# Kernel tuning notes

Measured on AMD Instinct MI355X. Metric: run time of the kernel, lower is better.

## Reference

```python
import jax, jax.numpy as jnp
import numpy as np

CLAMP = 1.0e6
LN_EPS = 1e-5
TWO_PI = 6.283185307179586


def _layernorm_last(x, gamma, beta):
    mu = jnp.mean(x, axis=-1, keepdims=True)
    var = jnp.var(x, axis=-1, keepdims=True)
    return (x - mu) * jax.lax.rsqrt(var + LN_EPS) * gamma + beta


def _candidates(xc):
    # xc: (C, B, S, D) pre-scaled + clamped input, one slice per candidate
    return jnp.stack([
        xc[0],
        xc[1] * xc[1],
        jnp.cos(TWO_PI * xc[2]),
        jnp.sin(xc[3]),
        jnp.exp(xc[4]),
        jnp.ones_like(xc[5]),
        xc[6] * xc[6] * xc[6],
        jnp.log(jnp.abs(xc[7]) + 1.0),
        jnp.sqrt(jnp.abs(xc[8])),
        jnp.tanh(xc[9]),
    ], axis=0)


def setup_inputs() -> dict:
    key = jax.random.key(0)
    ks = jax.random.split(key, 5)
    B, S, D, C = 4, 2048, 1024, 10
    return {
        "x": jax.random.normal(ks[0], (B, S, D), dtype=jnp.float32),
        "ln_gamma": jnp.ones((D,), dtype=jnp.float32),
        "ln_beta": jnp.zeros((D,), dtype=jnp.float32),
        "log_in_scale": jax.random.normal(ks[1], (C,), dtype=jnp.float32) * 0.05,
        "log_out_scale": jax.random.normal(ks[2], (C,), dtype=jnp.float32) * 0.05,
        "gate_w": jax.random.normal(ks[3], (C, D), dtype=jnp.float32) * (D ** -0.5),
        "gate_b": jnp.zeros((C,), dtype=jnp.float32),
    }


def reference(x, ln_gamma, ln_beta, log_in_scale, log_out_scale, gate_w, gate_b):
    # Input LayerNorm over D
    x_norm = _layernorm_last(x, ln_gamma, ln_beta)  # (B,S,D)

    in_s = jnp.exp(log_in_scale)    # (C,)
    out_s = jnp.exp(log_out_scale)  # (C,)

    # Per-candidate input scale + clamp
    xc = x_norm[None] * in_s[:, None, None, None]          # (C,B,S,D)
    xc = jnp.clip(xc, -CLAMP, CLAMP)

    cand = _candidates(xc) * out_s[:, None, None, None]    # (C,B,S,D)
    cand = jnp.clip(cand, -CLAMP, CLAMP)

    # permute to (B,S,C,D) and LayerNorm jointly over (C,D), no affine
    cand = jnp.transpose(cand, (1, 2, 0, 3))                # (B,S,C,D)
    mu = jnp.mean(cand, axis=(2, 3), keepdims=True)
    var = jnp.var(cand, axis=(2, 3), keepdims=True)
    cand = (cand - mu) * jax.lax.rsqrt(var + LN_EPS)
    cand = jnp.clip(cand, -CLAMP, CLAMP)
    cand = jnp.nan_to_num(cand, nan=0.0, posinf=CLAMP, neginf=-CLAMP)

    # Gate on the RAW input x (as in the torch code), softmax over candidates
    gate_logits = jnp.einsum('bsd,cd->bsc', x, gate_w) + gate_b  # (B,S,C)
    gate_weights = jax.nn.softmax(gate_logits, axis=-1)

    # Weighted sum over the candidate axis
    weighted = jnp.einsum('bsc,bscd->bsd', gate_weights, cand)   # (B,S,D)
    return weighted, gate_weights
```

## Files before the change

### kernel.cpp

```cpp
#include <hip/hip_runtime.h>
#include <math.h>

constexpr int D_DIM = 1024;
constexpr int C_DIM = 10;
constexpr int WPB   = 8;
constexpr int BLOCK = 64 * WPB;

constexpr float CLAMP_V  = 1.0e6f;
constexpr float LOG2E    = 1.4426950408889634f;
constexpr float LN2      = 0.6931471805599453f;
constexpr float INV_2PI  = 0.15915494309189535f;

__device__ __forceinline__ float2 pmul(float2 a, float2 b) {
    return make_float2(a.x * b.x, a.y * b.y);
}
__device__ __forceinline__ float2 pfma(float2 a, float2 b, float2 c) {
    return make_float2(fmaf(a.x, b.x, c.x), fmaf(a.y, b.y, c.y));
}
__device__ __forceinline__ float2 padd(float2 a, float2 b) {
    return make_float2(a.x + b.x, a.y + b.y);
}
__device__ __forceinline__ float2 bc(float s) { return make_float2(s, s); }

__device__ __forceinline__ float rfl(float x) {
    return __int_as_float(__builtin_amdgcn_readfirstlane(__float_as_int(x)));
}

template <int CTRL>
__device__ __forceinline__ float dpp_add(float v) {
    const int s = __builtin_amdgcn_update_dpp(
        0, __float_as_int(v), CTRL, 0xf, 0xf, false);
    return v + __int_as_float(s);
}
__device__ __forceinline__ float wave_sum_sgpr(float v) {
    v = dpp_add<0x111>(v);
    v = dpp_add<0x112>(v);
    v = dpp_add<0x114>(v);
    v = dpp_add<0x118>(v);
    v = dpp_add<0x142>(v);
    v = dpp_add<0x143>(v);
    return __int_as_float(__builtin_amdgcn_readlane(__float_as_int(v), 63));
}

__global__ __launch_bounds__(BLOCK)
void fused_sme_kernel(const float* __restrict__ x,
                      const float* __restrict__ ln_gamma,
                      const float* __restrict__ ln_beta,
                      const float* __restrict__ log_in_scale,
                      const float* __restrict__ log_out_scale,
                      const float* __restrict__ gate_w,
                      const float* __restrict__ gate_b,
                      float* __restrict__ out_weighted,
                      float* __restrict__ out_gate,
                      int tokens)
{
    const int t    = threadIdx.x;
    const int lane = t & 63;
    const int wv   = t >> 6;
    int token = blockIdx.x * WPB + wv;
    token = min(token, tokens - 1);

    __shared__ float gws[C_DIM * D_DIM];

    const float* xrow = x + (size_t)token * D_DIM + (lane << 2);
    float4 xv[4];
#pragma unroll
    for (int k = 0; k < 4; ++k)
        xv[k] = *reinterpret_cast<const float4*>(xrow + k * 256);

#pragma unroll
    for (int i = 0; i < 5; ++i) {
        const int idx = t + i * BLOCK;
        reinterpret_cast<float4*>(gws)[idx] =
            reinterpret_cast<const float4*>(gate_w)[idx];
    }

    float r[12];
    {
        float2 s = bc(0.0f), q = bc(0.0f);
#pragma unroll
        for (int k = 0; k < 4; ++k) {
            const float2 lo = make_float2(xv[k].x, xv[k].y);
            const float2 hi = make_float2(xv[k].z, xv[k].w);
            s = padd(s, padd(lo, hi));
            q = pfma(lo, lo, q);
            q = pfma(hi, hi, q);
        }
        r[0] = wave_sum_sgpr(s.x + s.y);
        r[1] = wave_sum_sgpr(q.x + q.y);
    }

    __syncthreads();

#pragma unroll
    for (int c = 0; c < C_DIM; ++c) {
        const float* gr = gws + c * D_DIM + (lane << 2);
        float2 d2 = bc(0.0f);
#pragma unroll
        for (int k = 0; k < 4; ++k) {
            const float4 gv = *reinterpret_cast<const float4*>(gr + k * 256);
            d2 = pfma(make_float2(xv[k].x, xv[k].y), make_float2(gv.x, gv.y), d2);
            d2 = pfma(make_float2(xv[k].z, xv[k].w), make_float2(gv.z, gv.w), d2);
        }
        r[2 + c] = wave_sum_sgpr(d2.x + d2.y);
    }

    __syncthreads();

    const float mu   = r[0] * (1.0f / D_DIM);
    const float var  = r[1] * (1.0f / D_DIM) - mu * mu;
    const float rstd = rfl(rsqrtf(var + 1e-5f));

    float w[C_DIM];
    float gmax = -3.4e38f;
#pragma unroll
    for (int c = 0; c < C_DIM; ++c) {
        w[c] = r[2 + c] + gate_b[c];
        gmax = fmaxf(gmax, w[c]);
    }
    float esum = 0.0f;
#pragma unroll
    for (int c = 0; c < C_DIM; ++c) {
        w[c] = __builtin_amdgcn_exp2f((w[c] - gmax) * LOG2E);
        esum += w[c];
    }
    const float rsum = __builtin_amdgcn_rcpf(esum);
#pragma unroll
    for (int c = 0; c < C_DIM; ++c) w[c] = rfl(w[c] * rsum);

    if (lane < C_DIM) out_gate[token * C_DIM + lane] = w[lane];

    float in_s[C_DIM], out_s[C_DIM];
#pragma unroll
    for (int c = 0; c < C_DIM; ++c) {
        in_s[c]  = __builtin_amdgcn_exp2f(log_in_scale[c]  * LOG2E);
        out_s[c] = __builtin_amdgcn_exp2f(log_out_scale[c] * LOG2E);
    }
    const float a0 = rfl(out_s[0] * in_s[0]);
    const float a1 = rfl(out_s[1] * in_s[1] * in_s[1]);
    const float k2 = rfl(in_s[2]),           o2 = rfl(out_s[2]);
    const float k3 = rfl(in_s[3] * INV_2PI), o3 = rfl(out_s[3]);
    const float k4 = rfl(in_s[4] * LOG2E),   o4 = rfl(out_s[4]);
    const float v5 = rfl(fminf(out_s[5], CLAMP_V));
    const float a6 = rfl(out_s[6] * in_s[6] * in_s[6] * in_s[6]);
    const float k7 = rfl(in_s[7]),           o7 = rfl(out_s[7] * LN2);
    const float k8 = rfl(in_s[8]),           o8 = rfl(out_s[8]);
    const float k9 = rfl(2.0f * in_s[9] * LOG2E);
    const float o9 = rfl(out_s[9]),          m9 = rfl(-2.0f * out_s[9]);

    float2 xn[8];
#pragma unroll
    for (int k = 0; k < 4; ++k) {
        const float4 gv = *reinterpret_cast<const float4*>(ln_gamma + k * 256 + (lane << 2));
        const float4 bv = *reinterpret_cast<const float4*>(ln_beta  + k * 256 + (lane << 2));
        const float2 zlo = pmul(padd(make_float2(xv[k].x, xv[k].y), bc(-mu)), bc(rstd));
        const float2 zhi = pmul(padd(make_float2(xv[k].z, xv[k].w), bc(-mu)), bc(rstd));
        xn[2 * k]     = pfma(zlo, make_float2(gv.x, gv.y), make_float2(bv.x, bv.y));
        xn[2 * k + 1] = pfma(zhi, make_float2(gv.z, gv.w), make_float2(bv.z, bv.w));
    }

    float2* accw = reinterpret_cast<float2*>(gws + (wv << 10));

    const float accbase = rfl(w[5] * v5);
    float2 S1 = bc(0.0f), S2 = bc(0.0f);

#pragma unroll
    for (int p = 0; p < 8; ++p) {
        const float2 xj = xn[p];
        const float2 ax = make_float2(fabsf(xj.x), fabsf(xj.y));
        const float2 x2 = pmul(xj, xj);

        const float2 v0 = pmul(bc(a0), xj);
        const float2 v1 = pmul(bc(a1), x2);

        float2 u2 = pmul(bc(k2), xj);
        u2 = padd(u2, make_float2(-rintf(u2.x), -rintf(u2.y)));
        const float2 v2 = pmul(bc(o2),
            make_float2(__builtin_amdgcn_cosf(u2.x), __builtin_amdgcn_cosf(u2.y)));

        float2 u3 = pmul(bc(k3), xj);
        u3 = padd(u3, make_float2(-rintf(u3.x), -rintf(u3.y)));
        const float2 v3 = pmul(bc(o3),
            make_float2(__builtin_amdgcn_sinf(u3.x), __builtin_amdgcn_sinf(u3.y)));

        const float2 u4 = pmul(bc(k4), xj);
        float2 v4 = pmul(bc(o4),
            make_float2(__builtin_amdgcn_exp2f(u4.x), __builtin_amdgcn_exp2f(u4.y)));
        v4 = make_float2(fminf(v4.x, CLAMP_V), fminf(v4.y, CLAMP_V));

        const float2 v6 = pmul(bc(a6), pmul(x2, xj));

        const float2 u7 = pfma(bc(k7), ax, bc(1.0f));
        const float2 v7 = pmul(bc(o7),
            make_float2(__builtin_amdgcn_logf(u7.x), __builtin_amdgcn_logf(u7.y)));

        const float2 u8 = pmul(bc(k8), ax);
        const float2 v8 = pmul(bc(o8),
            make_float2(__builtin_amdgcn_sqrtf(u8.x), __builtin_amdgcn_sqrtf(u8.y)));

        const float2 u9 = pmul(bc(k9), xj);
        const float2 e9 = padd(
            make_float2(__builtin_amdgcn_exp2f(u9.x), __builtin_amdgcn_exp2f(u9.y)),
            bc(1.0f));
        const float2 v9 = pfma(bc(m9),
            make_float2(__builtin_amdgcn_rcpf(e9.x), __builtin_amdgcn_rcpf(e9.y)),
            bc(o9));

        S1 = padd(S1, padd(padd(padd(v0, v1), padd(v2, v3)),
                           padd(padd(v4, v6), padd(padd(v7, v8), v9))));
        S2 = pfma(v0, v0, S2); S2 = pfma(v1, v1, S2); S2 = pfma(v2, v2, S2);
        S2 = pfma(v3, v3, S2); S2 = pfma(v4, v4, S2); S2 = pfma(v6, v6, S2);
        S2 = pfma(v7, v7, S2); S2 = pfma(v8, v8, S2); S2 = pfma(v9, v9, S2);

        float2 a = bc(accbase);
        a = pfma(bc(w[0]), v0, a); a = pfma(bc(w[1]), v1, a);
        a = pfma(bc(w[2]), v2, a); a = pfma(bc(w[3]), v3, a);
        a = pfma(bc(w[4]), v4, a); a = pfma(bc(w[6]), v6, a);
        a = pfma(bc(w[7]), v7, a); a = pfma(bc(w[8]), v8, a);
        a = pfma(bc(w[9]), v9, a);
        accw[(p << 6) + lane] = a;
    }

    const float s1 = wave_sum_sgpr(S1.x + S1.y + 16.0f * v5);
    const float s2 = wave_sum_sgpr(fmaf(16.0f * v5, v5, S2.x + S2.y));

    constexpr float rn = 1.0f / (float)(C_DIM * D_DIM);
    const float mu2  = s1 * rn;
    const float var2 = s2 * rn - mu2 * mu2;
    const float rsig = rfl(rsqrtf(var2 + 1e-5f));

    float* orow = out_weighted + (size_t)token * D_DIM + (lane << 2);
#pragma unroll
    for (int k = 0; k < 4; ++k) {
        const float2 lo = pmul(padd(accw[((2 * k)     << 6) + lane], bc(-mu2)), bc(rsig));
        const float2 hi = pmul(padd(accw[((2 * k + 1) << 6) + lane], bc(-mu2)), bc(rsig));
        float4 o;
        o.x = lo.x; o.y = lo.y; o.z = hi.x; o.w = hi.y;
        *reinterpret_cast<float4*>(orow + k * 256) = o;
    }
}

extern "C" void kernel_launch(void* const* d_in, const int* in_sizes, int n_in,
                              void* d_out, int out_size, void* d_ws, size_t ws_size,
                              hipStream_t stream) {
    const float* x   = (const float*)d_in[0];
    const float* lg  = (const float*)d_in[1];
    const float* lb  = (const float*)d_in[2];
    const float* lis = (const float*)d_in[3];
    const float* los = (const float*)d_in[4];
    const float* gw  = (const float*)d_in[5];
    const float* gb  = (const float*)d_in[6];

    const int tokens = in_sizes[0] / D_DIM;
    float* out      = (float*)d_out;
    float* out_gate = out + (size_t)tokens * D_DIM;

    const int grid = (tokens + WPB - 1) / WPB;
    hipLaunchKernelGGL(fused_sme_kernel, dim3(grid), dim3(BLOCK), 0, stream,
                       x, lg, lb, lis, los, gw, gb, out, out_gate, tokens);
}
```

Baseline: 30.49 us.

## Split fused kernel into stats/gate pass and candidate pass via workspace

Splits the single fused kernel into two launches. The first computes the LayerNorm statistics and the gate softmax, using the 40KB gate_w copy in shared memory, and writes them to a small workspace. The second re-reads x, has no shared memory, and keeps the candidate accumulators in registers instead of LDS, so it can reach higher occupancy for the transcendental-heavy part. The cost is an extra kernel launch and a second full read of x (16MB), which may well outweigh the occupancy gain.

```diff
diff --git a/kernel.cpp b/kernel.cpp
--- a/kernel.cpp
+++ b/kernel.cpp
@@ -3,8 +3,11 @@
 
 constexpr int D_DIM = 1024;
 constexpr int C_DIM = 10;
-constexpr int WPB   = 8;
-constexpr int BLOCK = 64 * WPB;
+constexpr int K1_WPB = 8;
+constexpr int K1_BLOCK = 64 * K1_WPB;
+constexpr int K2_WPB = 4;
+constexpr int K2_BLOCK = 64 * K2_WPB;
+constexpr int ST = 12;
 
 constexpr float CLAMP_V  = 1.0e6f;
 constexpr float LOG2E    = 1.4426950408889634f;
@@ -42,22 +45,18 @@
     return __int_as_float(__builtin_amdgcn_readlane(__float_as_int(v), 63));
 }
 
-__global__ __launch_bounds__(BLOCK)
-void fused_sme_kernel(const float* __restrict__ x,
-                      const float* __restrict__ ln_gamma,
-                      const float* __restrict__ ln_beta,
-                      const float* __restrict__ log_in_scale,
-                      const float* __restrict__ log_out_scale,
-                      const float* __restrict__ gate_w,
-                      const float* __restrict__ gate_b,
-                      float* __restrict__ out_weighted,
-                      float* __restrict__ out_gate,
-                      int tokens)
+__global__ __launch_bounds__(K1_BLOCK)
+void stats_kernel(const float* __restrict__ x,
+                  const float* __restrict__ gate_w,
+                  const float* __restrict__ gate_b,
+                  float* __restrict__ stats,
+                  float* __restrict__ out_gate,
+                  int tokens)
 {
     const int t    = threadIdx.x;
     const int lane = t & 63;
     const int wv   = t >> 6;
-    int token = blockIdx.x * WPB + wv;
+    int token = blockIdx.x * K1_WPB + wv;
     token = min(token, tokens - 1);
 
     __shared__ float gws[C_DIM * D_DIM];
@@ -70,7 +69,7 @@
 
 #pragma unroll
     for (int i = 0; i < 5; ++i) {
-        const int idx = t + i * BLOCK;
+        const int idx = t + i * K1_BLOCK;
         reinterpret_cast<float4*>(gws)[idx] =
             reinterpret_cast<const float4*>(gate_w)[idx];
     }
@@ -105,8 +104,6 @@
         r[2 + c] = wave_sum_sgpr(d2.x + d2.y);
     }
 
-    __syncthreads();
-
     const float mu   = r[0] * (1.0f / D_DIM);
     const float var  = r[1] * (1.0f / D_DIM) - mu * mu;
     const float rstd = rfl(rsqrtf(var + 1e-5f));
@@ -128,7 +125,43 @@
 #pragma unroll
     for (int c = 0; c < C_DIM; ++c) w[c] = rfl(w[c] * rsum);
 
-    if (lane < C_DIM) out_gate[token * C_DIM + lane] = w[lane];
+    if (lane < C_DIM) {
+        out_gate[token * C_DIM + lane] = w[lane];
+        stats[token * ST + lane] = w[lane];
+    }
+    if (lane == 0) {
+        stats[token * ST + 10] = mu;
+        stats[token * ST + 11] = rstd;
+    }
+}
+
+__global__ __launch_bounds__(K2_BLOCK)
+void cand_kernel(const float* __restrict__ x,
+                 const float* __restrict__ ln_gamma,
+                 const float* __restrict__ ln_beta,
+                 const float* __restrict__ log_in_scale,
+                 const float* __restrict__ log_out_scale,
+                 const float* __restrict__ stats,
+                 float* __restrict__ out_weighted,
+                 int tokens)
+{
+    const int lane = threadIdx.x & 63;
+    const int wv   = threadIdx.x >> 6;
+    int token = blockIdx.x * K2_WPB + wv;
+    token = min(token, tokens - 1);
+
+    const float* st = stats + token * ST;
+    float w[C_DIM];
+#pragma unroll
+    for (int c = 0; c < C_DIM; ++c) w[c] = st[c];
+    const float mu   = st[10];
+    const float rstd = st[11];
+
+    const float* xrow = x + (size_t)token * D_DIM + (lane << 2);
+    float4 xv[4];
+#pragma unroll
+    for (int k = 0; k < 4; ++k)
+        xv[k] = *reinterpret_cast<const float4*>(xrow + k * 256);
 
     float in_s[C_DIM], out_s[C_DIM];
 #pragma unroll
@@ -159,8 +192,6 @@
         xn[2 * k + 1] = pfma(zhi, make_float2(gv.z, gv.w), make_float2(bv.z, bv.w));
     }
 
-    float2* accw = reinterpret_cast<float2*>(gws + (wv << 10));
-
     const float accbase = rfl(w[5] * v5);
     float2 S1 = bc(0.0f), S2 = bc(0.0f);
 
@@ -218,7 +249,7 @@
         a = pfma(bc(w[4]), v4, a); a = pfma(bc(w[6]), v6, a);
         a = pfma(bc(w[7]), v7, a); a = pfma(bc(w[8]), v8, a);
         a = pfma(bc(w[9]), v9, a);
-        accw[(p << 6) + lane] = a;
+        xn[p] = a;
     }
 
     const float s1 = wave_sum_sgpr(S1.x + S1.y + 16.0f * v5);
@@ -232,8 +263,8 @@
     float* orow = out_weighted + (size_t)token * D_DIM + (lane << 2);
 #pragma unroll
     for (int k = 0; k < 4; ++k) {
-        const float2 lo = pmul(padd(accw[((2 * k)     << 6) + lane], bc(-mu2)), bc(rsig));
-        const float2 hi = pmul(padd(accw[((2 * k + 1) << 6) + lane], bc(-mu2)), bc(rsig));
+        const float2 lo = pmul(padd(xn[2 * k],     bc(-mu2)), bc(rsig));
+        const float2 hi = pmul(padd(xn[2 * k + 1], bc(-mu2)), bc(rsig));
         float4 o;
         o.x = lo.x; o.y = lo.y; o.z = hi.x; o.w = hi.y;
         *reinterpret_cast<float4*>(orow + k * 256) = o;
@@ -254,8 +285,13 @@
     const int tokens = in_sizes[0] / D_DIM;
     float* out      = (float*)d_out;
     float* out_gate = out + (size_t)tokens * D_DIM;
-
-    const int grid = (tokens + WPB - 1) / WPB;
-    hipLaunchKernelGGL(fused_sme_kernel, dim3(grid), dim3(BLOCK), 0, stream,
-                       x, lg, lb, lis, los, gw, gb, out, out_gate, tokens);
-}
+    float* stats    = (float*)d_ws;
+
+    const int g1 = (tokens + K1_WPB - 1) / K1_WPB;
+    hipLaunchKernelGGL(stats_kernel, dim3(g1), dim3(K1_BLOCK), 0, stream,
+                       x, gw, gb, stats, out_gate, tokens);
+
+    const int g2 = (tokens + K2_WPB - 1) / K2_WPB;
+    hipLaunchKernelGGL(cand_kernel, dim3(g2), dim3(K2_BLOCK), 0, stream,
+                       x, lg, lb, lis, los, stats, out, tokens);
+}
```

Result: slower. 31.77 us (+4.2%).
